# Kernel optimization log

Hardware: AMD Instinct MI355X
Metric: run time of the kernel (lower is better)

Reference implementation:

```python
import math
import jax, jax.numpy as jnp
import numpy as np

B, LD, LE = 4, 1024, 1024
D, H, DK, DV, DFF, NL = 256, 8, 32, 32, 1024, 6


def _fixed_pos_emb(L, d):
    inv_freq = 1.0 / (10000.0 ** (jnp.arange(0, d, 2, dtype=jnp.float32) / d))
    pos = jnp.arange(L, dtype=jnp.float32)
    s = pos[:, None] * inv_freq[None, :]          # [L, d/2]
    return jnp.concatenate([jnp.sin(s), jnp.cos(s)], axis=-1)  # [L, d]


def _ln(x, g, b, eps=1e-5):
    m = x.mean(-1, keepdims=True)
    v = x.var(-1, keepdims=True)
    return (x - m) / jnp.sqrt(v + eps) * g + b


def _mha(x_q, x_kv, Wq, bq, Wk, bk, Wv, bv, Wo, bo, g, b, mask):
    Bq, Lq, _ = x_q.shape
    q = (x_q @ Wq + bq).reshape(Bq, Lq, H, DK).transpose(0, 2, 1, 3)   # [B,H,Lq,DK]
    k = (x_kv @ Wk + bk).reshape(Bq, -1, H, DK).transpose(0, 2, 1, 3)  # [B,H,Lk,DK]
    v = (x_kv @ Wv + bv).reshape(Bq, -1, H, DV).transpose(0, 2, 1, 3)  # [B,H,Lk,DV]
    scores = jnp.einsum('bhqd,bhkd->bhqk', q, k) / math.sqrt(DK)
    scores = jnp.where(mask[:, None, :, :], -1e9, scores)
    attn = jax.nn.softmax(scores, axis=-1)
    ctx = jnp.einsum('bhqk,bhkd->bhqd', attn, v)
    ctx = ctx.transpose(0, 2, 1, 3).reshape(Bq, Lq, H * DV)
    return _ln(ctx @ Wo + bo + x_q, g, b)


def _ffn(x, W1, b1, W2, b2, g, b):
    h = jax.nn.relu(x @ W1 + b1)   # conv1d k=1 == pointwise linear
    return _ln(h @ W2 + b2 + x, g, b)


def setup_inputs() -> dict:
    key = jax.random.key(0)
    ks = iter(jax.random.split(key, 40))
    def p(shape):
        return jax.random.normal(next(ks), shape, jnp.float32) * 0.02
    inp = {
        'enc_outputs': jax.random.normal(next(ks), (B, LE, D), jnp.float32),
        'dec_inputs': jax.random.normal(next(ks), (B, LD, 3), jnp.float32),
        'enc_masks': jnp.zeros((B, LE), jnp.int32),
        'dec_masks': jnp.zeros((B, LD), jnp.int32),
        'W_tgt': p((3, D)), 'b_tgt': jnp.zeros((D,), jnp.float32),
        'sa_Wq': p((NL, D, H * DK)), 'sa_bq': jnp.zeros((NL, H * DK), jnp.float32),
        'sa_Wk': p((NL, D, H * DK)), 'sa_bk': jnp.zeros((NL, H * DK), jnp.float32),
        'sa_Wv': p((NL, D, H * DV)), 'sa_bv': jnp.zeros((NL, H * DV), jnp.float32),
        'sa_Wo': p((NL, H * DV, D)), 'sa_bo': jnp.zeros((NL, D), jnp.float32),
        'sa_ln_g': jnp.ones((NL, D), jnp.float32), 'sa_ln_b': jnp.zeros((NL, D), jnp.float32),
        'ca_Wq': p((NL, D, H * DK)), 'ca_bq': jnp.zeros((NL, H * DK), jnp.float32),
        'ca_Wk': p((NL, D, H * DK)), 'ca_bk': jnp.zeros((NL, H * DK), jnp.float32),
        'ca_Wv': p((NL, D, H * DV)), 'ca_bv': jnp.zeros((NL, H * DV), jnp.float32),
        'ca_Wo': p((NL, H * DV, D)), 'ca_bo': jnp.zeros((NL, D), jnp.float32),
        'ca_ln_g': jnp.ones((NL, D), jnp.float32), 'ca_ln_b': jnp.zeros((NL, D), jnp.float32),
        'ff_W1': p((NL, D, DFF)), 'ff_b1': jnp.zeros((NL, DFF), jnp.float32),
        'ff_W2': p((NL, DFF, D)), 'ff_b2': jnp.zeros((NL, D), jnp.float32),
        'ff_ln_g': jnp.ones((NL, D), jnp.float32), 'ff_ln_b': jnp.zeros((NL, D), jnp.float32),
    }
    return inp


def reference(enc_outputs, dec_inputs, enc_masks, dec_masks, W_tgt, b_tgt,
              sa_Wq, sa_bq, sa_Wk, sa_bk, sa_Wv, sa_bv, sa_Wo, sa_bo, sa_ln_g, sa_ln_b,
              ca_Wq, ca_bq, ca_Wk, ca_bk, ca_Wv, ca_bv, ca_Wo, ca_bo, ca_ln_g, ca_ln_b,
              ff_W1, ff_b1, ff_W2, ff_b2, ff_ln_g, ff_ln_b):
    x = dec_inputs @ W_tgt + b_tgt                                  # tgt_emb
    pad = dec_masks[:, None, :].astype(bool)                        # [B,1,LD]
    causal = jnp.triu(jnp.ones((LD, LD), bool), 1)[None]            # [1,LD,LD]
    self_mask = pad | causal                                        # [B,LD,LD]
    cross_mask = jnp.broadcast_to(enc_masks[:, None, :].astype(bool), (x.shape[0], LD, LE))
    pe = _fixed_pos_emb(LD, D)[None]                                # [1,LD,D]
    for i in range(NL):
        x = x + pe                                                  # pos emb applied every layer (as in source)
        x = _mha(x, x, sa_Wq[i], sa_bq[i], sa_Wk[i], sa_bk[i], sa_Wv[i], sa_bv[i],
                 sa_Wo[i], sa_bo[i], sa_ln_g[i], sa_ln_b[i], self_mask)
        x = _mha(x, enc_outputs, ca_Wq[i], ca_bq[i], ca_Wk[i], ca_bk[i], ca_Wv[i], ca_bv[i],
                 ca_Wo[i], ca_bo[i], ca_ln_g[i], ca_ln_b[i], cross_mask)
        x = _ffn(x, ff_W1[i], ff_b1[i], ff_W2[i], ff_b2[i], ff_ln_g[i], ff_ln_b[i])
    return x
```

## Files before the change

### kernel.cpp

```cpp
#include <hip/hip_runtime.h>
#include <hip/hip_bf16.h>

#define B_   4
#define LD_  1024
#define LE_  1024
#define D_   256
#define H_   8
#define DK_  32
#define DFF_ 1024
#define NL_  6
#define NTOK (B_ * LD_)
#define M1E  1048576

typedef __hip_bfloat16 bf16;
typedef __bf16 bf16_t;
typedef bf16_t bf16x8 __attribute__((ext_vector_type(8)));
typedef bf16_t bf16x4 __attribute__((ext_vector_type(4)));
typedef float  f32x4  __attribute__((ext_vector_type(4)));

__device__ __forceinline__ float bits2f(unsigned short u) {
    union { unsigned int i; float f; } w; w.i = ((unsigned int)u) << 16; return w.f;
}
__device__ __forceinline__ float ldx(const void* p, size_t i, int f32) {
    if (f32) return ((const float*)p)[i];
    return bits2f(((const unsigned short*)p)[i]);
}

__global__ __launch_bounds__(256) void detect_kernel(
    const void* __restrict__ enc, int* __restrict__ flag)
{
    __shared__ int bad;
    if (threadIdx.x == 0) bad = 0;
    __syncthreads();
    const unsigned short* u = (const unsigned short*)enc;
    int b = 0;
    for (int i = threadIdx.x; i < 4096; i += 256) {
        unsigned short e = (u[i] >> 7) & 0xFF;
        if (e >= 142) b = 1;
    }
    if (b) atomicOr(&bad, 1);
    __syncthreads();
    if (threadIdx.x == 0) *flag = bad;
}

__global__ __launch_bounds__(256) void pe_build_kernel(float* __restrict__ pe)
{
    int i = blockIdx.x * 256 + threadIdx.x;
    int d = i & (D_ - 1);
    int pos = i >> 8;
    int j = d & 127;
    float inv = powf(10000.0f, -2.0f * (float)j / (float)D_);
    float s = (float)pos * inv;
    pe[i] = (d < 128) ? sinf(s) : cosf(s);
}

__global__ __launch_bounds__(256) void embed_kernel(
    const void* __restrict__ dec, const void* __restrict__ Wt,
    const void* __restrict__ bt, float* __restrict__ x,
    const float* __restrict__ pe, const int* __restrict__ flag)
{
    int f32 = *flag;
    int i = blockIdx.x * 256 + threadIdx.x;
    int d = i & (D_ - 1);
    int t = i >> 8;
    float a0 = ldx(dec, t * 3 + 0, f32);
    float a1 = ldx(dec, t * 3 + 1, f32);
    float a2 = ldx(dec, t * 3 + 2, f32);
    x[i] = ldx(bt, d, f32) + a0 * ldx(Wt, 0 * D_ + d, f32)
         + a1 * ldx(Wt, 1 * D_ + d, f32) + a2 * ldx(Wt, 2 * D_ + d, f32)
         + pe[i & (LD_ * D_ - 1)];
}

__global__ __launch_bounds__(256) void conv_kernel(
    const void* __restrict__ in, float* __restrict__ out, const int* __restrict__ flag)
{
    int f32 = *flag;
    int i = blockIdx.x * 256 + threadIdx.x;
    out[i] = ldx(in, i, f32);
}

__global__ __launch_bounds__(256) void gemm3_kernel(
    const float* __restrict__ A0, const float* __restrict__ A1, const float* __restrict__ A2,
    const void* __restrict__ W0, const void* __restrict__ W1, const void* __restrict__ W2,
    const void* __restrict__ bias0, const void* __restrict__ bias1, const void* __restrict__ bias2,
    float* __restrict__ C0, float* __restrict__ C1, float* __restrict__ C2,
    size_t wOff, size_t bOff,
    int M, int N, int K, int relu, int mode, int aexact, const int* __restrict__ flag)
{
    const int f32 = *flag;
    const int z = blockIdx.z;
    const float* A = (z == 0) ? A0 : (z == 1) ? A1 : A2;
    const void*  W = (z == 0) ? W0 : (z == 1) ? W1 : W2;
    const void*  bias = (z == 0) ? bias0 : (z == 1) ? bias1 : bias2;
    float* C = (z == 0) ? C0 : (z == 1) ? C1 : C2;
    const int ax = (!f32 && aexact && z > 0);

    __shared__ __align__(16) bf16_t Ahi[32][40];
    __shared__ __align__(16) bf16_t Alo[32][40];
    __shared__ __align__(16) bf16_t Whi[64][40];
    __shared__ __align__(16) bf16_t Wlo[64][40];

    const int tid = threadIdx.x;
    const int m0 = blockIdx.y * 32, n0 = blockIdx.x * 64;
    const int w = tid >> 6, l = tid & 63, l15 = l & 15, lg = l >> 4;
    const int wr = w >> 1, wc = w & 1;

    const int ar = tid >> 3, ac = (tid & 7) * 4;
    const int wn = tid & 63, wkg = tid >> 6;
    const int wkb = 8 * (wkg ^ ((wn >> 3) & 3));

    const int fa = 16 * wr + l15;
    const int c0 = 32 * wc + l15, c1 = c0 + 16;
    const int kb0 = 8 * (lg ^ ((c0 >> 3) & 3));
    const int kb1 = 8 * (lg ^ ((c1 >> 3) & 3));

    f32x4 acc0 = {0.f, 0.f, 0.f, 0.f};
    f32x4 acc1 = {0.f, 0.f, 0.f, 0.f};

    float4 av = *(const float4*)&A[(size_t)(m0 + ar) * K + ac];
    float wf[8];
#pragma unroll
    for (int j = 0; j < 8; ++j)
        wf[j] = ldx(W, wOff + (size_t)(8 * wkg + j) * N + n0 + wn, f32);

    for (int k0 = 0; k0 < K; k0 += 32) {
        __syncthreads();
        {
            float af[4] = {av.x, av.y, av.z, av.w};
            bf16x4 h4, l4;
#pragma unroll
            for (int j = 0; j < 4; ++j) {
                bf16_t hv = (bf16_t)af[j];
                h4[j] = hv;
                l4[j] = (bf16_t)(af[j] - (float)hv);
            }
            *(bf16x4*)&Ahi[ar][ac] = h4;
            if (!ax) *(bf16x4*)&Alo[ar][ac] = l4;
            bf16x8 h8;
#pragma unroll
            for (int j = 0; j < 8; ++j) h8[j] = (bf16_t)wf[j];
            *(bf16x8*)&Whi[wn][wkb] = h8;
            if (f32) {
                bf16x8 l8;
#pragma unroll
                for (int j = 0; j < 8; ++j) l8[j] = (bf16_t)(wf[j] - (float)((bf16_t)wf[j]));
                *(bf16x8*)&Wlo[wn][wkb] = l8;
            }
        }
        __syncthreads();

        if (k0 + 32 < K) {
            av = *(const float4*)&A[(size_t)(m0 + ar) * K + k0 + 32 + ac];
#pragma unroll
            for (int j = 0; j < 8; ++j)
                wf[j] = ldx(W, wOff + (size_t)(k0 + 32 + 8 * wkg + j) * N + n0 + wn, f32);
        }

        bf16x8 ah = *(const bf16x8*)&Ahi[fa][8 * lg];
        bf16x8 bh0 = *(const bf16x8*)&Whi[c0][kb0];
        bf16x8 bh1 = *(const bf16x8*)&Whi[c1][kb1];
        acc0 = __builtin_amdgcn_mfma_f32_16x16x32_bf16(ah, bh0, acc0, 0, 0, 0);
        acc1 = __builtin_amdgcn_mfma_f32_16x16x32_bf16(ah, bh1, acc1, 0, 0, 0);
        if (!ax) {
            bf16x8 al = *(const bf16x8*)&Alo[fa][8 * lg];
            acc0 = __builtin_amdgcn_mfma_f32_16x16x32_bf16(al, bh0, acc0, 0, 0, 0);
            acc1 = __builtin_amdgcn_mfma_f32_16x16x32_bf16(al, bh1, acc1, 0, 0, 0);
        }
        if (f32) {
            bf16x8 bl0 = *(const bf16x8*)&Wlo[c0][kb0];
            bf16x8 bl1 = *(const bf16x8*)&Wlo[c1][kb1];
            acc0 = __builtin_amdgcn_mfma_f32_16x16x32_bf16(ah, bl0, acc0, 0, 0, 0);
            acc1 = __builtin_amdgcn_mfma_f32_16x16x32_bf16(ah, bl1, acc1, 0, 0, 0);
        }
    }

    const int cm = m0 + 16 * wr + 4 * lg;
    const int cn = n0 + 32 * wc + l15;
    const float b0v = ldx(bias, bOff + cn, f32);
    const float b1v = ldx(bias, bOff + cn + 16, f32);
    if (mode == 0) {
#pragma unroll
        for (int r = 0; r < 4; ++r) {
            float v0 = acc0[r] + b0v;
            float v1 = acc1[r] + b1v;
            if (relu) { v0 = fmaxf(v0, 0.f); v1 = fmaxf(v1, 0.f); }
            C[(size_t)(cm + r) * N + cn]      = v0;
            C[(size_t)(cm + r) * N + cn + 16] = v1;
        }
    } else {
        bf16_t* Cb = (bf16_t*)C;
        const float qs = (z == 0) ? 0.17677669529663687f : 1.0f;
#pragma unroll
        for (int r = 0; r < 4; ++r) {
            const int token = cm + r;
#pragma unroll
            for (int cc = 0; cc < 2; ++cc) {
                const int d = cn + 16 * cc;
                const float v = ((cc == 0 ? acc0[r] : acc1[r]) + (cc == 0 ? b0v : b1v)) * qs;
                if (z < 2) {
                    int bb = token >> 10, qw = (token >> 4) & 63, lt = token & 15;
                    int hh = d >> 5, lg2 = (d >> 3) & 3, jj = d & 7;
                    size_t base = ((size_t)((bb * 8 + hh) * 64 + qw)) * 1024
                                + (size_t)(lg2 * 16 + lt) * 8 + jj;
                    bf16_t hv = (bf16_t)v;
                    Cb[base]       = hv;
                    Cb[base + 512] = (bf16_t)(v - (float)hv);
                } else {
                    int bb = token >> 10, ktt = (token >> 6) & 15, c2 = (token >> 5) & 1;
                    int w32 = token & 31;
                    int lg2 = (w32 >> 2) & 3, jj = (w32 >> 4) * 4 + (w32 & 3);
                    int hh = d >> 5, dvh = (d >> 4) & 1, lt = d & 15;
                    size_t base = ((size_t)((bb * 8 + hh) * 16 + ktt)) * 2048
                                + c2 * 1024 + dvh * 512 + (size_t)(lg2 * 16 + lt) * 8 + jj;
                    Cb[base] = (bf16_t)v;
                }
            }
        }
    }
}

__global__ __launch_bounds__(1024) void gemmln_kernel(
    const float* __restrict__ A, const void* __restrict__ W,
    const void* __restrict__ bias, float* __restrict__ x,
    const void* __restrict__ g, const void* __restrict__ bt,
    size_t wOff, size_t bOff, int K,
    const float* __restrict__ pe, int addpe, const int* __restrict__ flag)
{
    const int f32 = *flag;
    __shared__ __align__(16) bf16_t Ahi[16][40];
    __shared__ __align__(16) bf16_t Alo[16][40];
    __shared__ __align__(16) bf16_t Whi[256][40];
    __shared__ __align__(16) bf16_t Wlo[256][40];
    __shared__ float red1[16][16];
    __shared__ float red2[16][16];
    __shared__ float mrow[16], irow[16];

    const int tid = threadIdx.x;
    const int m0 = blockIdx.x * 16;
    const int w = tid >> 6, l = tid & 63, l15 = l & 15, lg = l >> 4;

    const int ar = tid >> 3, ac = (tid & 7) * 4;
    const int wn = tid & 255, wkg = tid >> 8;
    const int wkb = 8 * (wkg ^ ((wn >> 3) & 3));
    const int c = 16 * w + l15;
    const int kb = 8 * (lg ^ ((c >> 3) & 3));

    f32x4 acc = {0.f, 0.f, 0.f, 0.f};

    float4 av;
    float wf[8];
    if (tid < 128) av = *(const float4*)&A[(size_t)(m0 + ar) * K + ac];
#pragma unroll
    for (int j = 0; j < 8; ++j)
        wf[j] = ldx(W, wOff + (size_t)(8 * wkg + j) * 256 + wn, f32);

    for (int k0 = 0; k0 < K; k0 += 32) {
        __syncthreads();
        if (tid < 128) {
            float af[4] = {av.x, av.y, av.z, av.w};
            bf16x4 h4, l4;
#pragma unroll
            for (int j = 0; j < 4; ++j) {
                bf16_t hv = (bf16_t)af[j];
                h4[j] = hv;
                l4[j] = (bf16_t)(af[j] - (float)hv);
            }
            *(bf16x4*)&Ahi[ar][ac] = h4;
            *(bf16x4*)&Alo[ar][ac] = l4;
        }
        {
            bf16x8 h8;
#pragma unroll
            for (int j = 0; j < 8; ++j) h8[j] = (bf16_t)wf[j];
            *(bf16x8*)&Whi[wn][wkb] = h8;
            if (f32) {
                bf16x8 l8;
#pragma unroll
                for (int j = 0; j < 8; ++j) l8[j] = (bf16_t)(wf[j] - (float)((bf16_t)wf[j]));
                *(bf16x8*)&Wlo[wn][wkb] = l8;
            }
        }
        __syncthreads();

        if (k0 + 32 < K) {
            if (tid < 128) av = *(const float4*)&A[(size_t)(m0 + ar) * K + k0 + 32 + ac];
#pragma unroll
            for (int j = 0; j < 8; ++j)
                wf[j] = ldx(W, wOff + (size_t)(k0 + 32 + 8 * wkg + j) * 256 + wn, f32);
        }

        bf16x8 ah = *(const bf16x8*)&Ahi[l15][8 * lg];
        bf16x8 bh = *(const bf16x8*)&Whi[c][kb];
        acc = __builtin_amdgcn_mfma_f32_16x16x32_bf16(ah, bh, acc, 0, 0, 0);
        {
            bf16x8 al = *(const bf16x8*)&Alo[l15][8 * lg];
            acc = __builtin_amdgcn_mfma_f32_16x16x32_bf16(al, bh, acc, 0, 0, 0);
        }
        if (f32) {
            bf16x8 bl = *(const bf16x8*)&Wlo[c][kb];
            acc = __builtin_amdgcn_mfma_f32_16x16x32_bf16(ah, bl, acc, 0, 0, 0);
        }
    }

    const float bv = ldx(bias, bOff + c, f32);
    f32x4 v;
    float s1[4], s2[4];
#pragma unroll
    for (int r = 0; r < 4; ++r) {
        int tok = m0 + 4 * lg + r;
        v[r] = acc[r] + bv + x[(size_t)tok * 256 + c];
        s1[r] = v[r];
        s2[r] = v[r] * v[r];
    }
#pragma unroll
    for (int r = 0; r < 4; ++r) {
        s1[r] += __shfl_xor(s1[r], 1);  s2[r] += __shfl_xor(s2[r], 1);
        s1[r] += __shfl_xor(s1[r], 2);  s2[r] += __shfl_xor(s2[r], 2);
        s1[r] += __shfl_xor(s1[r], 4);  s2[r] += __shfl_xor(s2[r], 4);
        s1[r] += __shfl_xor(s1[r], 8);  s2[r] += __shfl_xor(s2[r], 8);
    }
    if (l15 == 0) {
#pragma unroll
        for (int r = 0; r < 4; ++r) {
            red1[w][4 * lg + r] = s1[r];
            red2[w][4 * lg + r] = s2[r];
        }
    }
    __syncthreads();
    if (tid < 16) {
        float t1 = 0.f, t2 = 0.f;
#pragma unroll
        for (int ww = 0; ww < 16; ++ww) { t1 += red1[ww][tid]; t2 += red2[ww][tid]; }
        float mean = t1 * (1.0f / 256.0f);
        float var  = t2 * (1.0f / 256.0f) - mean * mean;
        mrow[tid] = mean;
        irow[tid] = 1.0f / sqrtf(var + 1e-5f);
    }
    __syncthreads();

    const float gv  = ldx(g,  bOff + c, f32);
    const float btv = ldx(bt, bOff + c, f32);
#pragma unroll
    for (int r = 0; r < 4; ++r) {
        int row = 4 * lg + r;
        int tok = m0 + row;
        float out = (v[r] - mrow[row]) * irow[row] * gv + btv;
        if (addpe) out += pe[(size_t)(tok & (LD_ - 1)) * 256 + c];
        x[(size_t)tok * 256 + c] = out;
    }
}

__global__ __launch_bounds__(256) void fattn4_kernel(
    const bf16_t* __restrict__ Qf, const bf16_t* __restrict__ Kf,
    const bf16_t* __restrict__ Vf, float* __restrict__ O,
    const int* __restrict__ mask, int causal)
{
    const int tid = threadIdx.x;
    const int qt = (int)blockIdx.x ^ ((((int)blockIdx.z >> 1) & 1) << 3);
    const int h = blockIdx.y, b = blockIdx.z;
    const int w = tid >> 6, l = tid & 63, l15 = l & 15, lg = l >> 4;
    const int bh = b * H_ + h;

    const size_t qbase = ((size_t)(bh * 64 + qt * 4 + w)) * 1024 + l * 8;
    const bf16x8 qh = *(const bf16x8*)(Qf + qbase);
    const bf16x8 ql = *(const bf16x8*)(Qf + qbase + 512);
    const int q_global = qt * 64 + w * 16 + l15;

    const bf16_t* kp = Kf + (size_t)bh * 64 * 1024 + l * 8;
    const bf16_t* vp = Vf + (size_t)bh * 16 * 2048 + l * 8;
    const int*    mp = mask + b * 1024 + 4 * lg;

    float m = -3.0e38f, lsum = 0.0f;
    f32x4 o0 = {0.f, 0.f, 0.f, 0.f};
    f32x4 o1 = {0.f, 0.f, 0.f, 0.f};

    const int nkt = causal ? (qt + 1) : (LE_ / 64);

    bf16x8 kha[4], kla[4], vaa[4];  int4 mka[4];
    bf16x8 khb[4], klb[4], vab[4];  int4 mkb[4];

#define FA_LOAD(kh_, kl_, va_, mk_, KT) do {                                    \
    _Pragma("unroll")                                                           \
    for (int nt = 0; nt < 4; ++nt) {                                            \
        kh_[nt] = *(const bf16x8*)(kp + (size_t)(KT) * 4096 + nt * 1024);       \
        kl_[nt] = *(const bf16x8*)(kp + (size_t)(KT) * 4096 + nt * 1024 + 512); \
    }                                                                           \
    va_[0] = *(const bf16x8*)(vp + (size_t)(KT) * 2048);                        \
    va_[1] = *(const bf16x8*)(vp + (size_t)(KT) * 2048 + 1024);                 \
    va_[2] = *(const bf16x8*)(vp + (size_t)(KT) * 2048 + 512);                  \
    va_[3] = *(const bf16x8*)(vp + (size_t)(KT) * 2048 + 1536);                 \
    _Pragma("unroll")                                                           \
    for (int nt = 0; nt < 4; ++nt)                                              \
        mk_[nt] = *(const int4*)(mp + (KT) * 64 + nt * 16);                     \
} while (0)

#define FA_COMPUTE(kh_, kl_, va_, mk_, KT) do {                                 \
    f32x4 s[4];                                                                 \
    _Pragma("unroll")                                                           \
    for (int nt = 0; nt < 4; ++nt) {                                            \
        f32x4 acc = {0.f, 0.f, 0.f, 0.f};                                       \
        acc = __builtin_amdgcn_mfma_f32_16x16x32_bf16(kh_[nt], qh, acc, 0,0,0); \
        acc = __builtin_amdgcn_mfma_f32_16x16x32_bf16(kl_[nt], qh, acc, 0,0,0); \
        acc = __builtin_amdgcn_mfma_f32_16x16x32_bf16(kh_[nt], ql, acc, 0,0,0); \
        s[nt] = acc;                                                            \
    }                                                                           \
    float pm = -3.0e38f;                                                        \
    _Pragma("unroll")                                                           \
    for (int nt = 0; nt < 4; ++nt) {                                            \
        _Pragma("unroll")                                                       \
        for (int r = 0; r < 4; ++r) {                                           \
            int key = (KT) * 64 + 16 * nt + 4 * lg + r;                         \
            int mv = (r==0)?mk_[nt].x:(r==1)?mk_[nt].y:(r==2)?mk_[nt].z:mk_[nt].w; \
            bool dead = (mv != 0) || (causal && key > q_global);                \
            float v = dead ? -1e30f : s[nt][r];                                 \
            s[nt][r] = v;                                                       \
            pm = fmaxf(pm, v);                                                  \
        }                                                                       \
    }                                                                           \
    pm = fmaxf(pm, __shfl_xor(pm, 16));                                         \
    pm = fmaxf(pm, __shfl_xor(pm, 32));                                         \
    float mnew = fmaxf(m, pm);                                                  \
    float alpha = __expf(m - mnew);                                             \
    m = mnew;                                                                   \
    float psum = 0.f;                                                           \
    _Pragma("unroll")                                                           \
    for (int nt = 0; nt < 4; ++nt) {                                            \
        _Pragma("unroll")                                                       \
        for (int r = 0; r < 4; ++r) {                                           \
            float p = __expf(s[nt][r] - m);                                     \
            s[nt][r] = p;                                                       \
            psum += p;                                                          \
        }                                                                       \
    }                                                                           \
    psum += __shfl_xor(psum, 16);                                               \
    psum += __shfl_xor(psum, 32);                                               \
    lsum = lsum * alpha + psum;                                                 \
    _Pragma("unroll")                                                           \
    for (int r = 0; r < 4; ++r) { o0[r] *= alpha; o1[r] *= alpha; }             \
    bf16x8 pb0, pb1;                                                            \
    _Pragma("unroll")                                                           \
    for (int r = 0; r < 4; ++r) {                                               \
        pb0[r]     = (bf16_t)s[0][r];  pb0[4 + r] = (bf16_t)s[1][r];            \
        pb1[r]     = (bf16_t)s[2][r];  pb1[4 + r] = (bf16_t)s[3][r];            \
    }                                                                           \
    o0 = __builtin_amdgcn_mfma_f32_16x16x32_bf16(va_[0], pb0, o0, 0, 0, 0);     \
    o0 = __builtin_amdgcn_mfma_f32_16x16x32_bf16(va_[1], pb1, o0, 0, 0, 0);     \
    o1 = __builtin_amdgcn_mfma_f32_16x16x32_bf16(va_[2], pb0, o1, 0, 0, 0);     \
    o1 = __builtin_amdgcn_mfma_f32_16x16x32_bf16(va_[3], pb1, o1, 0, 0, 0);     \
} while (0)

    FA_LOAD(kha, kla, vaa, mka, 0);
    int kt = 0;
    for (; kt + 2 <= nkt; kt += 2) {
        FA_LOAD(khb, klb, vab, mkb, kt + 1);
        FA_COMPUTE(kha, kla, vaa, mka, kt);
        if (kt + 2 < nkt) FA_LOAD(kha, kla, vaa, mka, kt + 2);
        FA_COMPUTE(khb, klb, vab, mkb, kt + 1);
    }
    if (kt < nkt) FA_COMPUTE(kha, kla, vaa, mka, kt);

#undef FA_LOAD
#undef FA_COMPUTE

    const float inv = 1.0f / lsum;
    float* op = O + ((size_t)(b * LD_ + q_global)) * D_ + h * DK_ + 4 * lg;
    f32x4 r0, r1;
#pragma unroll
    for (int r = 0; r < 4; ++r) { r0[r] = o0[r] * inv; r1[r] = o1[r] * inv; }
    *(f32x4*)op = r0;
    *(f32x4*)(op + 16) = r1;
}

__global__ __launch_bounds__(256) void cast_kernel(
    const float* __restrict__ x, void* __restrict__ out, const int* __restrict__ flag)
{
    int f32 = *flag;
    int i = blockIdx.x * 256 + threadIdx.x;
    if (f32) ((float*)out)[i] = x[i];
    else ((bf16*)out)[i] = __float2bfloat16(x[i]);
}

extern "C" void kernel_launch(void* const* d_in, const int* in_sizes, int n_in,
                              void* d_out, int out_size, void* d_ws, size_t ws_size,
                              hipStream_t stream)
{
    const void* enc       = d_in[0];
    const void* dec       = d_in[1];
    const int*  enc_masks = (const int*)d_in[2];
    const int*  dec_masks = (const int*)d_in[3];
    const void* W_tgt = d_in[4];
    const void* b_tgt = d_in[5];
    const void* sa_Wq = d_in[6];
    const void* sa_bq = d_in[7];
    const void* sa_Wk = d_in[8];
    const void* sa_bk = d_in[9];
    const void* sa_Wv = d_in[10];
    const void* sa_bv = d_in[11];
    const void* sa_Wo = d_in[12];
    const void* sa_bo = d_in[13];
    const void* sa_ln_g = d_in[14];
    const void* sa_ln_b = d_in[15];
    const void* ca_Wq = d_in[16];
    const void* ca_bq = d_in[17];
    const void* ca_Wk = d_in[18];
    const void* ca_bk = d_in[19];
    const void* ca_Wv = d_in[20];
    const void* ca_bv = d_in[21];
    const void* ca_Wo = d_in[22];
    const void* ca_bo = d_in[23];
    const void* ca_ln_g = d_in[24];
    const void* ca_ln_b = d_in[25];
    const void* ff_W1 = d_in[26];
    const void* ff_b1 = d_in[27];
    const void* ff_W2 = d_in[28];
    const void* ff_b2 = d_in[29];
    const void* ff_ln_g = d_in[30];
    const void* ff_ln_b = d_in[31];

    const size_t M1 = (size_t)NTOK * D_;
    float* ws = (float*)d_ws;
    float* x     = ws;
    float* t     = ws + 1 * M1;
    float* ctx   = ws + 2 * M1;
    float* enc_f = ws + 3 * M1;
    float* h     = ws + 4 * M1;
    bf16_t* qbuf = (bf16_t*)(ws + 4 * M1);
    bf16_t* kbuf = (bf16_t*)(ws + 5 * M1);
    bf16_t* vtbuf= (bf16_t*)(ws + 6 * M1);
    float* pe    = ws + 8 * M1;
    int*   flag  = (int*)(ws + 9 * M1);

    const int nElem = NTOK * D_;
    (void)t;

    detect_kernel<<<1, 256, 0, stream>>>(enc, flag);
    pe_build_kernel<<<(LD_ * D_) / 256, 256, 0, stream>>>(pe);
    embed_kernel<<<nElem / 256, 256, 0, stream>>>(dec, W_tgt, b_tgt, x, pe, flag);
    conv_kernel<<<nElem / 256, 256, 0, stream>>>(enc, enc_f, flag);

    dim3 gProj(D_ / 64, NTOK / 32, 3);
    dim3 gFF1(DFF_ / 64, NTOK / 32, 1);
    dim3 gAttn(LD_ / 64, H_, B_);

    for (int i = 0; i < NL_; ++i) {
        const size_t wOff  = (size_t)i * D_ * D_;
        const size_t bOff  = (size_t)i * D_;
        const size_t f1Off = (size_t)i * D_ * DFF_;
        const size_t f1bOff= (size_t)i * DFF_;

        gemm3_kernel<<<gProj, 256, 0, stream>>>(
            x, x, x, sa_Wq, sa_Wk, sa_Wv, sa_bq, sa_bk, sa_bv,
            (float*)qbuf, (float*)kbuf, (float*)vtbuf,
            wOff, bOff, NTOK, D_, D_, 0, 1, 0, flag);
        fattn4_kernel<<<gAttn, 256, 0, stream>>>(qbuf, kbuf, vtbuf, ctx, dec_masks, 1);
        gemmln_kernel<<<NTOK / 16, 1024, 0, stream>>>(
            ctx, sa_Wo, sa_bo, x, sa_ln_g, sa_ln_b, wOff, bOff, D_, pe, 0, flag);

        gemm3_kernel<<<gProj, 256, 0, stream>>>(
            x, enc_f, enc_f, ca_Wq, ca_Wk, ca_Wv, ca_bq, ca_bk, ca_bv,
            (float*)qbuf, (float*)kbuf, (float*)vtbuf,
            wOff, bOff, NTOK, D_, D_, 0, 1, 1, flag);
        fattn4_kernel<<<gAttn, 256, 0, stream>>>(qbuf, kbuf, vtbuf, ctx, enc_masks, 0);
        gemmln_kernel<<<NTOK / 16, 1024, 0, stream>>>(
            ctx, ca_Wo, ca_bo, x, ca_ln_g, ca_ln_b, wOff, bOff, D_, pe, 0, flag);

        gemm3_kernel<<<gFF1, 256, 0, stream>>>(
            x, x, x, ff_W1, ff_W1, ff_W1, ff_b1, ff_b1, ff_b1,
            h, h, h, f1Off, f1bOff, NTOK, DFF_, D_, 1, 0, 0, flag);
        gemmln_kernel<<<NTOK / 16, 1024, 0, stream>>>(
            h, ff_W2, ff_b2, x, ff_ln_g, ff_ln_b, f1Off, bOff, DFF_,
            pe, (i < NL_ - 1) ? 1 : 0, flag);
    }

    cast_kernel<<<nElem / 256, 256, 0, stream>>>(x, d_out, flag);
}
```

Baseline: 1.107 ms.

## Pre-swizzle weights into MFMA fragment layout and keep activations as bf16 hi/lo pairs

Adds a one-time prep kernel that converts every layer's weights into bf16 hi/lo pairs stored in the MFMA fragment order, so the GEMM kernels can load B operands directly from global memory without LDS staging or __syncthreads. Producers (embed, attention output, LN epilogue, FFN1) now write activations already split into bf16 hi/lo pairs, which removes the per-tile float-to-bf16 conversion in every GEMM. The FFN hidden buffer is stored as bf16 pairs rather than fp32. The cost is a larger workspace, extra conversion passes per call, and GEMMs that read operands straight from global memory with less explicit reuse across waves.

```diff
diff --git a/kernel.cpp b/kernel.cpp
--- a/kernel.cpp
+++ b/kernel.cpp
@@ -11,6 +11,7 @@
 #define NL_  6
 #define NTOK (B_ * LD_)
 #define M1E  1048576
+#define WTOT 6291456
 
 typedef __hip_bfloat16 bf16;
 typedef __bf16 bf16_t;
@@ -43,6 +44,48 @@
     if (threadIdx.x == 0) *flag = bad;
 }
 
+__global__ __launch_bounds__(256) void prep_w_kernel(
+    const void* sWq, const void* sWk, const void* sWv, const void* sWo,
+    const void* cWq, const void* cWk, const void* cWv, const void* cWo,
+    const void* fW1, const void* fW2,
+    bf16_t* __restrict__ Wf, const int* __restrict__ flag)
+{
+    const int f32 = *flag;
+    const int g = blockIdx.x * 256 + threadIdx.x;
+    const int li = g >> 17;
+    int r = g & 131071;
+    const void* src;
+    size_t so;
+    int N;
+    if (r < 65536) {
+        int t = r >> 13; r &= 8191;
+        N = 256; so = (size_t)li * 65536;
+        if      (t == 0) src = sWq; else if (t == 1) src = sWk;
+        else if (t == 2) src = sWv; else if (t == 3) src = sWo;
+        else if (t == 4) src = cWq; else if (t == 5) src = cWk;
+        else if (t == 6) src = cWv; else             src = cWo;
+    } else if (r < 98304) {
+        r -= 65536; N = 1024; so = (size_t)li * 262144; src = fW1;
+    } else {
+        r -= 98304; N = 256;  so = (size_t)li * 262144; src = fW2;
+    }
+    const int lane = r & 63;
+    const int q2 = r >> 6;
+    int nb, kb;
+    if (N == 256) { nb = q2 & 15; kb = q2 >> 4; }
+    else          { nb = q2 & 63; kb = q2 >> 6; }
+    const int k = kb * 32 + 8 * (lane >> 4);
+    const int n = nb * 16 + (lane & 15);
+    const size_t out = (size_t)g * 8;
+#pragma unroll
+    for (int j = 0; j < 8; ++j) {
+        float v = ldx(src, so + (size_t)(k + j) * N + n, f32);
+        bf16_t hv = (bf16_t)v;
+        Wf[out + j] = hv;
+        if (f32) Wf[WTOT + out + j] = (bf16_t)(v - (float)hv);
+    }
+}
+
 __global__ __launch_bounds__(256) void pe_build_kernel(float* __restrict__ pe)
 {
     int i = blockIdx.x * 256 + threadIdx.x;
@@ -57,6 +100,7 @@
 __global__ __launch_bounds__(256) void embed_kernel(
     const void* __restrict__ dec, const void* __restrict__ Wt,
     const void* __restrict__ bt, float* __restrict__ x,
+    bf16_t* __restrict__ xhi, bf16_t* __restrict__ xlo,
     const float* __restrict__ pe, const int* __restrict__ flag)
 {
     int f32 = *flag;
@@ -66,109 +110,78 @@
     float a0 = ldx(dec, t * 3 + 0, f32);
     float a1 = ldx(dec, t * 3 + 1, f32);
     float a2 = ldx(dec, t * 3 + 2, f32);
-    x[i] = ldx(bt, d, f32) + a0 * ldx(Wt, 0 * D_ + d, f32)
-         + a1 * ldx(Wt, 1 * D_ + d, f32) + a2 * ldx(Wt, 2 * D_ + d, f32)
-         + pe[i & (LD_ * D_ - 1)];
-}
-
-__global__ __launch_bounds__(256) void conv_kernel(
-    const void* __restrict__ in, float* __restrict__ out, const int* __restrict__ flag)
+    float v = ldx(bt, d, f32) + a0 * ldx(Wt, 0 * D_ + d, f32)
+            + a1 * ldx(Wt, 1 * D_ + d, f32) + a2 * ldx(Wt, 2 * D_ + d, f32)
+            + pe[i & (LD_ * D_ - 1)];
+    x[i] = v;
+    bf16_t hv = (bf16_t)v;
+    xhi[i] = hv;
+    xlo[i] = (bf16_t)(v - (float)hv);
+}
+
+__global__ __launch_bounds__(256) void enc_split_kernel(
+    const void* __restrict__ in, bf16_t* __restrict__ ehi, bf16_t* __restrict__ elo,
+    const int* __restrict__ flag)
 {
     int f32 = *flag;
     int i = blockIdx.x * 256 + threadIdx.x;
-    out[i] = ldx(in, i, f32);
-}
-
-__global__ __launch_bounds__(256) void gemm3_kernel(
-    const float* __restrict__ A0, const float* __restrict__ A1, const float* __restrict__ A2,
-    const void* __restrict__ W0, const void* __restrict__ W1, const void* __restrict__ W2,
-    const void* __restrict__ bias0, const void* __restrict__ bias1, const void* __restrict__ bias2,
-    float* __restrict__ C0, float* __restrict__ C1, float* __restrict__ C2,
-    size_t wOff, size_t bOff,
-    int M, int N, int K, int relu, int mode, int aexact, const int* __restrict__ flag)
+    float v = ldx(in, i, f32);
+    bf16_t hv = (bf16_t)v;
+    ehi[i] = hv;
+    elo[i] = (bf16_t)(v - (float)hv);
+}
+
+__global__ __launch_bounds__(256) void gemmf_kernel(
+    const bf16_t* __restrict__ Ah0, const bf16_t* __restrict__ Al0,
+    const bf16_t* __restrict__ Ah1, const bf16_t* __restrict__ Al1,
+    const bf16_t* __restrict__ Ah2, const bf16_t* __restrict__ Al2,
+    const bf16_t* __restrict__ Wf, size_t wfBase, size_t wzStr,
+    const void* __restrict__ b0, const void* __restrict__ b1,
+    const void* __restrict__ b2, size_t bOff,
+    bf16_t* __restrict__ C0, bf16_t* __restrict__ C1,
+    bf16_t* __restrict__ C2, bf16_t* __restrict__ Cl,
+    int M, int N, int K, int mode, int aexact, const int* __restrict__ flag)
 {
     const int f32 = *flag;
     const int z = blockIdx.z;
-    const float* A = (z == 0) ? A0 : (z == 1) ? A1 : A2;
-    const void*  W = (z == 0) ? W0 : (z == 1) ? W1 : W2;
-    const void*  bias = (z == 0) ? bias0 : (z == 1) ? bias1 : bias2;
-    float* C = (z == 0) ? C0 : (z == 1) ? C1 : C2;
+    const bf16_t* Ah = (z == 0) ? Ah0 : (z == 1) ? Ah1 : Ah2;
+    const bf16_t* Al = (z == 0) ? Al0 : (z == 1) ? Al1 : Al2;
+    const void* bias = (z == 0) ? b0 : (z == 1) ? b1 : b2;
+    bf16_t* Cb = (z == 0) ? C0 : (z == 1) ? C1 : C2;
     const int ax = (!f32 && aexact && z > 0);
-
-    __shared__ __align__(16) bf16_t Ahi[32][40];
-    __shared__ __align__(16) bf16_t Alo[32][40];
-    __shared__ __align__(16) bf16_t Whi[64][40];
-    __shared__ __align__(16) bf16_t Wlo[64][40];
 
     const int tid = threadIdx.x;
     const int m0 = blockIdx.y * 32, n0 = blockIdx.x * 64;
     const int w = tid >> 6, l = tid & 63, l15 = l & 15, lg = l >> 4;
     const int wr = w >> 1, wc = w & 1;
 
-    const int ar = tid >> 3, ac = (tid & 7) * 4;
-    const int wn = tid & 63, wkg = tid >> 6;
-    const int wkb = 8 * (wkg ^ ((wn >> 3) & 3));
-
-    const int fa = 16 * wr + l15;
-    const int c0 = 32 * wc + l15, c1 = c0 + 16;
-    const int kb0 = 8 * (lg ^ ((c0 >> 3) & 3));
-    const int kb1 = 8 * (lg ^ ((c1 >> 3) & 3));
+    const bf16_t* wfp = Wf + wfBase + (size_t)z * wzStr;
+    const bf16_t* wlp = wfp + WTOT;
+    const int nbT = N >> 4;
+    const int nb0 = (n0 >> 4) + 2 * wc;
+
+    const bf16_t* ap  = Ah + (size_t)(m0 + 16 * wr + l15) * K + 8 * lg;
+    const bf16_t* alp = Al + (size_t)(m0 + 16 * wr + l15) * K + 8 * lg;
 
     f32x4 acc0 = {0.f, 0.f, 0.f, 0.f};
     f32x4 acc1 = {0.f, 0.f, 0.f, 0.f};
-
-    float4 av = *(const float4*)&A[(size_t)(m0 + ar) * K + ac];
-    float wf[8];
-#pragma unroll
-    for (int j = 0; j < 8; ++j)
-        wf[j] = ldx(W, wOff + (size_t)(8 * wkg + j) * N + n0 + wn, f32);
-
-    for (int k0 = 0; k0 < K; k0 += 32) {
-        __syncthreads();
-        {
-            float af[4] = {av.x, av.y, av.z, av.w};
-            bf16x4 h4, l4;
-#pragma unroll
-            for (int j = 0; j < 4; ++j) {
-                bf16_t hv = (bf16_t)af[j];
-                h4[j] = hv;
-                l4[j] = (bf16_t)(af[j] - (float)hv);
-            }
-            *(bf16x4*)&Ahi[ar][ac] = h4;
-            if (!ax) *(bf16x4*)&Alo[ar][ac] = l4;
-            bf16x8 h8;
-#pragma unroll
-            for (int j = 0; j < 8; ++j) h8[j] = (bf16_t)wf[j];
-            *(bf16x8*)&Whi[wn][wkb] = h8;
-            if (f32) {
-                bf16x8 l8;
-#pragma unroll
-                for (int j = 0; j < 8; ++j) l8[j] = (bf16_t)(wf[j] - (float)((bf16_t)wf[j]));
-                *(bf16x8*)&Wlo[wn][wkb] = l8;
-            }
-        }
-        __syncthreads();
-
-        if (k0 + 32 < K) {
-            av = *(const float4*)&A[(size_t)(m0 + ar) * K + k0 + 32 + ac];
-#pragma unroll
-            for (int j = 0; j < 8; ++j)
-                wf[j] = ldx(W, wOff + (size_t)(k0 + 32 + 8 * wkg + j) * N + n0 + wn, f32);
-        }
-
-        bf16x8 ah = *(const bf16x8*)&Ahi[fa][8 * lg];
-        bf16x8 bh0 = *(const bf16x8*)&Whi[c0][kb0];
-        bf16x8 bh1 = *(const bf16x8*)&Whi[c1][kb1];
+    const int K32 = K >> 5;
+
+#pragma unroll 2
+    for (int kb = 0; kb < K32; ++kb) {
+        bf16x8 ah  = *(const bf16x8*)(ap + kb * 32);
+        bf16x8 bh0 = *(const bf16x8*)(wfp + ((size_t)(kb * nbT + nb0) * 64 + l) * 8);
+        bf16x8 bh1 = *(const bf16x8*)(wfp + ((size_t)(kb * nbT + nb0 + 1) * 64 + l) * 8);
         acc0 = __builtin_amdgcn_mfma_f32_16x16x32_bf16(ah, bh0, acc0, 0, 0, 0);
         acc1 = __builtin_amdgcn_mfma_f32_16x16x32_bf16(ah, bh1, acc1, 0, 0, 0);
         if (!ax) {
-            bf16x8 al = *(const bf16x8*)&Alo[fa][8 * lg];
-            acc0 = __builtin_amdgcn_mfma_f32_16x16x32_bf16(al, bh0, acc0, 0, 0, 0);
-            acc1 = __builtin_amdgcn_mfma_f32_16x16x32_bf16(al, bh1, acc1, 0, 0, 0);
+            bf16x8 al8 = *(const bf16x8*)(alp + kb * 32);
+            acc0 = __builtin_amdgcn_mfma_f32_16x16x32_bf16(al8, bh0, acc0, 0, 0, 0);
+            acc1 = __builtin_amdgcn_mfma_f32_16x16x32_bf16(al8, bh1, acc1, 0, 0, 0);
         }
         if (f32) {
-            bf16x8 bl0 = *(const bf16x8*)&Wlo[c0][kb0];
-            bf16x8 bl1 = *(const bf16x8*)&Wlo[c1][kb1];
+            bf16x8 bl0 = *(const bf16x8*)(wlp + ((size_t)(kb * nbT + nb0) * 64 + l) * 8);
+            bf16x8 bl1 = *(const bf16x8*)(wlp + ((size_t)(kb * nbT + nb0 + 1) * 64 + l) * 8);
             acc0 = __builtin_amdgcn_mfma_f32_16x16x32_bf16(ah, bl0, acc0, 0, 0, 0);
             acc1 = __builtin_amdgcn_mfma_f32_16x16x32_bf16(ah, bl1, acc1, 0, 0, 0);
         }
@@ -178,17 +191,20 @@
     const int cn = n0 + 32 * wc + l15;
     const float b0v = ldx(bias, bOff + cn, f32);
     const float b1v = ldx(bias, bOff + cn + 16, f32);
-    if (mode == 0) {
+    if (mode == 2) {
 #pragma unroll
         for (int r = 0; r < 4; ++r) {
-            float v0 = acc0[r] + b0v;
-            float v1 = acc1[r] + b1v;
-            if (relu) { v0 = fmaxf(v0, 0.f); v1 = fmaxf(v1, 0.f); }
-            C[(size_t)(cm + r) * N + cn]      = v0;
-            C[(size_t)(cm + r) * N + cn + 16] = v1;
+#pragma unroll
+            for (int cc = 0; cc < 2; ++cc) {
+                float v = (cc == 0 ? acc0[r] : acc1[r]) + (cc == 0 ? b0v : b1v);
+                v = fmaxf(v, 0.0f);
+                size_t idx = (size_t)(cm + r) * N + cn + 16 * cc;
+                bf16_t hv = (bf16_t)v;
+                C0[idx] = hv;
+                Cl[idx] = (bf16_t)(v - (float)hv);
+            }
         }
     } else {
-        bf16_t* Cb = (bf16_t*)C;
         const float qs = (z == 0) ? 0.17677669529663687f : 1.0f;
 #pragma unroll
         for (int r = 0; r < 4; ++r) {
@@ -220,17 +236,15 @@
 }
 
 __global__ __launch_bounds__(1024) void gemmln_kernel(
-    const float* __restrict__ A, const void* __restrict__ W,
+    const bf16_t* __restrict__ Ah, const bf16_t* __restrict__ Al,
+    const bf16_t* __restrict__ Wf, size_t wfBase,
     const void* __restrict__ bias, float* __restrict__ x,
+    bf16_t* __restrict__ xhi, bf16_t* __restrict__ xlo,
     const void* __restrict__ g, const void* __restrict__ bt,
-    size_t wOff, size_t bOff, int K,
+    size_t bOff, int K,
     const float* __restrict__ pe, int addpe, const int* __restrict__ flag)
 {
     const int f32 = *flag;
-    __shared__ __align__(16) bf16_t Ahi[16][40];
-    __shared__ __align__(16) bf16_t Alo[16][40];
-    __shared__ __align__(16) bf16_t Whi[256][40];
-    __shared__ __align__(16) bf16_t Wlo[256][40];
     __shared__ float red1[16][16];
     __shared__ float red2[16][16];
     __shared__ float mrow[16], irow[16];
@@ -239,69 +253,30 @@
     const int m0 = blockIdx.x * 16;
     const int w = tid >> 6, l = tid & 63, l15 = l & 15, lg = l >> 4;
 
-    const int ar = tid >> 3, ac = (tid & 7) * 4;
-    const int wn = tid & 255, wkg = tid >> 8;
-    const int wkb = 8 * (wkg ^ ((wn >> 3) & 3));
-    const int c = 16 * w + l15;
-    const int kb = 8 * (lg ^ ((c >> 3) & 3));
+    const bf16_t* ap  = Ah + (size_t)(m0 + l15) * K + 8 * lg;
+    const bf16_t* alp = Al + (size_t)(m0 + l15) * K + 8 * lg;
+    const bf16_t* wfp = Wf + wfBase;
+    const bf16_t* wlp = wfp + WTOT;
 
     f32x4 acc = {0.f, 0.f, 0.f, 0.f};
-
-    float4 av;
-    float wf[8];
-    if (tid < 128) av = *(const float4*)&A[(size_t)(m0 + ar) * K + ac];
-#pragma unroll
-    for (int j = 0; j < 8; ++j)
-        wf[j] = ldx(W, wOff + (size_t)(8 * wkg + j) * 256 + wn, f32);
-
-    for (int k0 = 0; k0 < K; k0 += 32) {
-        __syncthreads();
-        if (tid < 128) {
-            float af[4] = {av.x, av.y, av.z, av.w};
-            bf16x4 h4, l4;
-#pragma unroll
-            for (int j = 0; j < 4; ++j) {
-                bf16_t hv = (bf16_t)af[j];
-                h4[j] = hv;
-                l4[j] = (bf16_t)(af[j] - (float)hv);
-            }
-            *(bf16x4*)&Ahi[ar][ac] = h4;
-            *(bf16x4*)&Alo[ar][ac] = l4;
-        }
-        {
-            bf16x8 h8;
-#pragma unroll
-            for (int j = 0; j < 8; ++j) h8[j] = (bf16_t)wf[j];
-            *(bf16x8*)&Whi[wn][wkb] = h8;
-            if (f32) {
-                bf16x8 l8;
-#pragma unroll
-                for (int j = 0; j < 8; ++j) l8[j] = (bf16_t)(wf[j] - (float)((bf16_t)wf[j]));
-                *(bf16x8*)&Wlo[wn][wkb] = l8;
-            }
-        }
-        __syncthreads();
-
-        if (k0 + 32 < K) {
-            if (tid < 128) av = *(const float4*)&A[(size_t)(m0 + ar) * K + k0 + 32 + ac];
-#pragma unroll
-            for (int j = 0; j < 8; ++j)
-                wf[j] = ldx(W, wOff + (size_t)(k0 + 32 + 8 * wkg + j) * 256 + wn, f32);
-        }
-
-        bf16x8 ah = *(const bf16x8*)&Ahi[l15][8 * lg];
-        bf16x8 bh = *(const bf16x8*)&Whi[c][kb];
+    const int K32 = K >> 5;
+
+#pragma unroll 2
+    for (int kb = 0; kb < K32; ++kb) {
+        bf16x8 ah = *(const bf16x8*)(ap + kb * 32);
+        bf16x8 bh = *(const bf16x8*)(wfp + ((size_t)(kb * 16 + w) * 64 + l) * 8);
         acc = __builtin_amdgcn_mfma_f32_16x16x32_bf16(ah, bh, acc, 0, 0, 0);
         {
-            bf16x8 al = *(const bf16x8*)&Alo[l15][8 * lg];
-            acc = __builtin_amdgcn_mfma_f32_16x16x32_bf16(al, bh, acc, 0, 0, 0);
+            bf16x8 al8 = *(const bf16x8*)(alp + kb * 32);
+            acc = __builtin_amdgcn_mfma_f32_16x16x32_bf16(al8, bh, acc, 0, 0, 0);
         }
         if (f32) {
-            bf16x8 bl = *(const bf16x8*)&Wlo[c][kb];
+            bf16x8 bl = *(const bf16x8*)(wlp + ((size_t)(kb * 16 + w) * 64 + l) * 8);
             acc = __builtin_amdgcn_mfma_f32_16x16x32_bf16(ah, bl, acc, 0, 0, 0);
         }
     }
 
+    const int c = 16 * w + l15;
     const float bv = ldx(bias, bOff + c, f32);
     f32x4 v;
     float s1[4], s2[4];
@@ -346,13 +321,18 @@
         int tok = m0 + row;
         float out = (v[r] - mrow[row]) * irow[row] * gv + btv;
         if (addpe) out += pe[(size_t)(tok & (LD_ - 1)) * 256 + c];
-        x[(size_t)tok * 256 + c] = out;
+        size_t idx = (size_t)tok * 256 + c;
+        x[idx] = out;
+        bf16_t hv = (bf16_t)out;
+        xhi[idx] = hv;
+        xlo[idx] = (bf16_t)(out - (float)hv);
     }
 }
 
 __global__ __launch_bounds__(256) void fattn4_kernel(
     const bf16_t* __restrict__ Qf, const bf16_t* __restrict__ Kf,
-    const bf16_t* __restrict__ Vf, float* __restrict__ O,
+    const bf16_t* __restrict__ Vf,
+    bf16_t* __restrict__ Chi, bf16_t* __restrict__ Clo,
     const int* __restrict__ mask, int causal)
 {
     const int tid = threadIdx.x;
@@ -463,12 +443,21 @@
 #undef FA_COMPUTE
 
     const float inv = 1.0f / lsum;
-    float* op = O + ((size_t)(b * LD_ + q_global)) * D_ + h * DK_ + 4 * lg;
-    f32x4 r0, r1;
-#pragma unroll
-    for (int r = 0; r < 4; ++r) { r0[r] = o0[r] * inv; r1[r] = o1[r] * inv; }
-    *(f32x4*)op = r0;
-    *(f32x4*)(op + 16) = r1;
+    bf16x4 h0, l0, h1, l1;
+#pragma unroll
+    for (int r = 0; r < 4; ++r) {
+        float f0 = o0[r] * inv;
+        float f1 = o1[r] * inv;
+        bf16_t hv0 = (bf16_t)f0;
+        bf16_t hv1 = (bf16_t)f1;
+        h0[r] = hv0;  l0[r] = (bf16_t)(f0 - (float)hv0);
+        h1[r] = hv1;  l1[r] = (bf16_t)(f1 - (float)hv1);
+    }
+    const size_t ob = ((size_t)(b * LD_ + q_global)) * 256 + h * DK_ + 4 * lg;
+    *(bf16x4*)(Chi + ob)      = h0;
+    *(bf16x4*)(Chi + ob + 16) = h1;
+    *(bf16x4*)(Clo + ob)      = l0;
+    *(bf16x4*)(Clo + ob + 16) = l1;
 }
 
 __global__ __launch_bounds__(256) void cast_kernel(
@@ -519,57 +508,65 @@
 
     const size_t M1 = (size_t)NTOK * D_;
     float* ws = (float*)d_ws;
-    float* x     = ws;
-    float* t     = ws + 1 * M1;
-    float* ctx   = ws + 2 * M1;
-    float* enc_f = ws + 3 * M1;
-    float* h     = ws + 4 * M1;
-    bf16_t* qbuf = (bf16_t*)(ws + 4 * M1);
-    bf16_t* kbuf = (bf16_t*)(ws + 5 * M1);
-    bf16_t* vtbuf= (bf16_t*)(ws + 6 * M1);
-    float* pe    = ws + 8 * M1;
-    int*   flag  = (int*)(ws + 9 * M1);
+    float*  x      = ws;
+    bf16_t* xhi    = (bf16_t*)(ws + 1 * M1);
+    bf16_t* xlo    = xhi + M1E;
+    bf16_t* ctxhi  = (bf16_t*)(ws + 2 * M1);
+    bf16_t* ctxlo  = ctxhi + M1E;
+    bf16_t* enchi  = (bf16_t*)(ws + 3 * M1);
+    bf16_t* enclo  = enchi + M1E;
+    bf16_t* hhi    = (bf16_t*)(ws + 4 * M1);
+    bf16_t* hlo    = (bf16_t*)(ws + 6 * M1);
+    bf16_t* qbuf   = (bf16_t*)(ws + 8 * M1);
+    bf16_t* kbuf   = (bf16_t*)(ws + 9 * M1);
+    bf16_t* vtbuf  = (bf16_t*)(ws + 10 * M1);
+    float*  pe     = ws + 10 * M1 + M1 / 2;
+    int*    flag   = (int*)(ws + 10 * M1 + 3 * M1 / 4);
+    bf16_t* Wf     = (bf16_t*)(ws + 11 * M1);
 
     const int nElem = NTOK * D_;
-    (void)t;
 
     detect_kernel<<<1, 256, 0, stream>>>(enc, flag);
+    prep_w_kernel<<<3072, 256, 0, stream>>>(
+        sa_Wq, sa_Wk, sa_Wv, sa_Wo, ca_Wq, ca_Wk, ca_Wv, ca_Wo,
+        ff_W1, ff_W2, Wf, flag);
     pe_build_kernel<<<(LD_ * D_) / 256, 256, 0, stream>>>(pe);
-    embed_kernel<<<nElem / 256, 256, 0, stream>>>(dec, W_tgt, b_tgt, x, pe, flag);
-    conv_kernel<<<nElem / 256, 256, 0, stream>>>(enc, enc_f, flag);
+    embed_kernel<<<nElem / 256, 256, 0, stream>>>(dec, W_tgt, b_tgt, x, xhi, xlo, pe, flag);
+    enc_split_kernel<<<nElem / 256, 256, 0, stream>>>(enc, enchi, enclo, flag);
 
     dim3 gProj(D_ / 64, NTOK / 32, 3);
     dim3 gFF1(DFF_ / 64, NTOK / 32, 1);
     dim3 gAttn(LD_ / 64, H_, B_);
 
     for (int i = 0; i < NL_; ++i) {
-        const size_t wOff  = (size_t)i * D_ * D_;
-        const size_t bOff  = (size_t)i * D_;
-        const size_t f1Off = (size_t)i * D_ * DFF_;
-        const size_t f1bOff= (size_t)i * DFF_;
-
-        gemm3_kernel<<<gProj, 256, 0, stream>>>(
-            x, x, x, sa_Wq, sa_Wk, sa_Wv, sa_bq, sa_bk, sa_bv,
-            (float*)qbuf, (float*)kbuf, (float*)vtbuf,
-            wOff, bOff, NTOK, D_, D_, 0, 1, 0, flag);
-        fattn4_kernel<<<gAttn, 256, 0, stream>>>(qbuf, kbuf, vtbuf, ctx, dec_masks, 1);
+        const size_t LB   = (size_t)i * 1048576;
+        const size_t bOff = (size_t)i * D_;
+
+        gemmf_kernel<<<gProj, 256, 0, stream>>>(
+            xhi, xlo, xhi, xlo, xhi, xlo,
+            Wf, LB, 65536, sa_bq, sa_bk, sa_bv, bOff,
+            qbuf, kbuf, vtbuf, nullptr, NTOK, D_, D_, 1, 0, flag);
+        fattn4_kernel<<<gAttn, 256, 0, stream>>>(qbuf, kbuf, vtbuf, ctxhi, ctxlo, dec_masks, 1);
         gemmln_kernel<<<NTOK / 16, 1024, 0, stream>>>(
-            ctx, sa_Wo, sa_bo, x, sa_ln_g, sa_ln_b, wOff, bOff, D_, pe, 0, flag);
-
-        gemm3_kernel<<<gProj, 256, 0, stream>>>(
-            x, enc_f, enc_f, ca_Wq, ca_Wk, ca_Wv, ca_bq, ca_bk, ca_bv,
-            (float*)qbuf, (float*)kbuf, (float*)vtbuf,
-            wOff, bOff, NTOK, D_, D_, 0, 1, 1, flag);
-        fattn4_kernel<<<gAttn, 256, 0, stream>>>(qbuf, kbuf, vtbuf, ctx, enc_masks, 0);
+            ctxhi, ctxlo, Wf, LB + 3 * 65536, sa_bo, x, xhi, xlo,
+            sa_ln_g, sa_ln_b, bOff, D_, pe, 0, flag);
+
+        gemmf_kernel<<<gProj, 256, 0, stream>>>(
+            xhi, xlo, enchi, enclo, enchi, enclo,
+            Wf, LB + 4 * 65536, 65536, ca_bq, ca_bk, ca_bv, bOff,
+            qbuf, kbuf, vtbuf, nullptr, NTOK, D_, D_, 1, 1, flag);
+        fattn4_kernel<<<gAttn, 256, 0, stream>>>(qbuf, kbuf, vtbuf, ctxhi, ctxlo, enc_masks, 0);
         gemmln_kernel<<<NTOK / 16, 1024, 0, stream>>>(
-            ctx, ca_Wo, ca_bo, x, ca_ln_g, ca_ln_b, wOff, bOff, D_, pe, 0, flag);
-
-        gemm3_kernel<<<gFF1, 256, 0, stream>>>(
-            x, x, x, ff_W1, ff_W1, ff_W1, ff_b1, ff_b1, ff_b1,
-            h, h, h, f1Off, f1bOff, NTOK, DFF_, D_, 1, 0, 0, flag);
+            ctxhi, ctxlo, Wf, LB + 7 * 65536, ca_bo, x, xhi, xlo,
+            ca_ln_g, ca_ln_b, bOff, D_, pe, 0, flag);
+
+        gemmf_kernel<<<gFF1, 256, 0, stream>>>(
+            xhi, xlo, xhi, xlo, xhi, xlo,
+            Wf, LB + 524288, 0, ff_b1, ff_b1, ff_b1, (size_t)i * DFF_,
+            hhi, hhi, hhi, hlo, NTOK, DFF_, D_, 2, 0, flag);
         gemmln_kernel<<<NTOK / 16, 1024, 0, stream>>>(
-            h, ff_W2, ff_b2, x, ff_ln_g, ff_ln_b, f1Off, bOff, DFF_,
-            pe, (i < NL_ - 1) ? 1 : 0, flag);
+            hhi, hlo, Wf, LB + 786432, ff_b2, x, xhi, xlo,
+            ff_ln_g, ff_ln_b, bOff, DFF_, pe, (i < NL_ - 1) ? 1 : 0, flag);
     }
 
     cast_kernel<<<nElem / 256, 256, 0, stream>>>(x, d_out, flag);
```

New measurement: 1.333 ms. 20.5% more time.
